# Kernel optimization log

Hardware: AMD Instinct MI355X
Metric: run time of the kernel (lower is better)

## Reference

```python
import jax, jax.numpy as jnp
import numpy as np

D_M = 1024
VOCAB = 50257
BASE = 10000.0
B, S = 8, 4096


def setup_inputs() -> dict:
    key = jax.random.key(0)
    k1, k2 = jax.random.split(key)
    x = jax.random.randint(k1, (B, S), 0, VOCAB, dtype=jnp.int64)
    emb_table = jax.random.normal(k2, (VOCAB, D_M), dtype=jnp.float32)
    return {"x": x, "emb_table": emb_table}


def _positional_encoding(seq_len, d_m, base, dtype):
    # Vectorized version of the original Python loop over d_m/2:
    # denoms[:, i] = arange(seq_len) / base**(2*i/d_m); even cols sin, odd cols cos.
    pos = jnp.arange(seq_len, dtype=dtype)                    # [S]
    i = jnp.arange(d_m // 2, dtype=dtype)                     # [D/2]
    inv_freq = jnp.power(jnp.asarray(base, dtype), -2.0 * i / d_m)  # [D/2]
    ang = pos[:, None] * inv_freq[None, :]                    # [S, D/2]
    pe = jnp.stack([jnp.sin(ang), jnp.cos(ang)], axis=-1)     # [S, D/2, 2]
    return pe.reshape(seq_len, d_m)                           # interleaved sin/cos


def reference(x, emb_table):
    # Embedding gather: [B, S] -> [B, S, D]
    emb = emb_table[x]
    pe = _positional_encoding(x.shape[1], emb_table.shape[1], BASE, emb_table.dtype)
    return emb + pe[None, :, :]
```

## Files before the change

### kernel.cpp

```cpp
#include <hip/hip_runtime.h>
#include <math.h>


#define D_M 1024
#define SEQ 4096

__global__ __launch_bounds__(256) void SinusoidalEmbedding_83030307766274_kernel(
    const int* __restrict__ x,
    const float* __restrict__ emb_table,
    float* __restrict__ out)
{
    const int t  = blockIdx.x;
    const int d4 = threadIdx.x;
    const int s  = t & (SEQ - 1);

    const int row = x[t];
    const float4* __restrict__ src = (const float4*)(emb_table + (size_t)row * D_M);
    float4 v = src[d4];

    const float c = -2.0f * 13.28771237954945f / (float)D_M;
    const float i0 = (float)(2 * d4);
    const float f0 = exp2f(i0 * c);
    const float f1 = exp2f((i0 + 1.0f) * c);
    const float sp = (float)s;

    float s0, c0, s1, c1;
    sincosf(sp * f0, &s0, &c0);
    sincosf(sp * f1, &s1, &c1);

    v.x += s0;
    v.y += c0;
    v.z += s1;
    v.w += c1;

    ((float4*)out)[(size_t)t * (D_M / 4) + d4] = v;
}

extern "C" void kernel_launch(void* const* d_in, const int* in_sizes, int n_in,
                              void* d_out, int out_size, void* d_ws, size_t ws_size,
                              hipStream_t stream)
{
    const int*   x         = (const int*)d_in[0];
    const float* emb_table = (const float*)d_in[1];
    float*       out       = (float*)d_out;

    const int n_tokens = in_sizes[0];
    SinusoidalEmbedding_83030307766274_kernel<<<n_tokens, 256, 0, stream>>>(x, emb_table, out);
}
```

Measured before the change: 302.1 us.

## Process all batch rows per position block and use hardware sin/cos

Result: no change. 306.7 us (+1.5%).

```diff
diff --git a/kernel.cpp b/kernel.cpp
--- a/kernel.cpp
+++ b/kernel.cpp
@@ -2,38 +2,52 @@
 #include <math.h>
 
 
-#define D_M 1024
-#define SEQ 4096
+#define D_M   1024
+#define SEQ   4096
+#define BATCH 8
 
 __global__ __launch_bounds__(256) void SinusoidalEmbedding_83030307766274_kernel(
     const int* __restrict__ x,
     const float* __restrict__ emb_table,
     float* __restrict__ out)
 {
-    const int t  = blockIdx.x;
+    const int s  = blockIdx.x;
     const int d4 = threadIdx.x;
-    const int s  = t & (SEQ - 1);
 
-    const int row = x[t];
-    const float4* __restrict__ src = (const float4*)(emb_table + (size_t)row * D_M);
-    float4 v = src[d4];
-
-    const float c = -2.0f * 13.28771237954945f / (float)D_M;
+    const float c      = -2.0f * 13.28771237954945f / (float)D_M;
+    const float inv2pi = 0.15915494309189535f;
     const float i0 = (float)(2 * d4);
-    const float f0 = exp2f(i0 * c);
-    const float f1 = exp2f((i0 + 1.0f) * c);
+    const float f0 = exp2f(i0 * c) * inv2pi;
+    const float f1 = exp2f((i0 + 1.0f) * c) * inv2pi;
     const float sp = (float)s;
 
-    float s0, c0, s1, c1;
-    sincosf(sp * f0, &s0, &c0);
-    sincosf(sp * f1, &s1, &c1);
+    float r0 = __builtin_amdgcn_fractf(sp * f0);
+    float r1 = __builtin_amdgcn_fractf(sp * f1);
+    float pe_x = __builtin_amdgcn_sinf(r0);
+    float pe_y = __builtin_amdgcn_cosf(r0);
+    float pe_z = __builtin_amdgcn_sinf(r1);
+    float pe_w = __builtin_amdgcn_cosf(r1);
 
-    v.x += s0;
-    v.y += c0;
-    v.z += s1;
-    v.w += c1;
+    int rows[BATCH];
+#pragma unroll
+    for (int b = 0; b < BATCH; ++b)
+        rows[b] = x[b * SEQ + s];
 
-    ((float4*)out)[(size_t)t * (D_M / 4) + d4] = v;
+    float4 v[BATCH];
+#pragma unroll
+    for (int b = 0; b < BATCH; ++b)
+        v[b] = ((const float4*)(emb_table + (size_t)rows[b] * D_M))[d4];
+
+    float4* __restrict__ o4 = (float4*)out;
+#pragma unroll
+    for (int b = 0; b < BATCH; ++b) {
+        float4 o = v[b];
+        o.x += pe_x;
+        o.y += pe_y;
+        o.z += pe_z;
+        o.w += pe_w;
+        o4[((size_t)b * SEQ + s) * (D_M / 4) + d4] = o;
+    }
 }
 
 extern "C" void kernel_launch(void* const* d_in, const int* in_sizes, int n_in,
@@ -44,6 +58,5 @@
     const float* emb_table = (const float*)d_in[1];
     float*       out       = (float*)d_out;
 
-    const int n_tokens = in_sizes[0];
-    SinusoidalEmbedding_83030307766274_kernel<<<n_tokens, 256, 0, stream>>>(x, emb_table, out);
+    SinusoidalEmbedding_83030307766274_kernel<<<SEQ, 256, 0, stream>>>(x, emb_table, out);
 }
```
